# Performance work log

Measured on AMD Instinct MI355X. Metric: run time of the kernel, lower is better.

## Reference

```python
import jax, jax.numpy as jnp
import numpy as np

DIM = 1024
NUM_HEADS = 16
HEAD_DIM = DIM // NUM_HEADS
SCALE = HEAD_DIM ** -0.5


def setup_inputs() -> dict:
    key = jax.random.key(0)
    k1, k2, k3 = jax.random.split(key, 3)
    B, N = 2, 2048
    x = jax.random.normal(k1, (B, N, DIM), dtype=jnp.float32)
    # qkv: Linear(dim, 3*dim, bias=False); proj: Linear(dim, dim) with bias
    w_qkv = jax.random.normal(k2, (3 * DIM, DIM), dtype=jnp.float32) * (DIM ** -0.5)
    w_proj = jax.random.normal(k3, (DIM, DIM), dtype=jnp.float32) * (DIM ** -0.5)
    b_proj = jnp.zeros((DIM,), dtype=jnp.float32)
    return {"x": x, "w_qkv": w_qkv, "w_proj": w_proj, "b_proj": b_proj}


def reference(x, w_qkv, w_proj, b_proj):
    B, N, C = x.shape
    H, D = NUM_HEADS, HEAD_DIM
    qkv = jnp.einsum('bnc,fc->bnf', x, w_qkv)                 # [B,N,3C]
    qkv = qkv.reshape(B, N, 3, H, D).transpose(2, 0, 3, 1, 4)  # [3,B,H,N,D]
    q, k, v = qkv[0], qkv[1], qkv[2]
    q = q * SCALE
    attn = jnp.einsum('bhnd,bhmd->bhnm', q, k)                 # [B,H,N,N]
    attn = jax.nn.softmax(attn, axis=-1)
    out = jnp.einsum('bhnm,bhmd->bhnd', attn, v)               # [B,H,N,D]
    out = out.transpose(0, 2, 1, 3).reshape(B, N, C)
    out = jnp.einsum('bnc,fc->bnf', out, w_proj) + b_proj
    return out
```

## Files before the change

### kernel.cpp

```cpp
#include <hip/hip_runtime.h>
#include <hip/hip_bf16.h>
#include <stdint.h>

typedef __attribute__((ext_vector_type(4))) float f32x4;
typedef __attribute__((ext_vector_type(16))) float f32x16;
typedef __attribute__((ext_vector_type(8))) short bf16x8;
typedef __attribute__((ext_vector_type(4))) short bf16x4;
typedef unsigned short ushort_t;

#define QSCALE 0.18033688f

__device__ inline short f2bf(float f) {
  unsigned u = __builtin_bit_cast(unsigned, f);
  u += 0x7fffu + ((u >> 16) & 1u);
  return (short)(u >> 16);
}

__device__ inline void gload_lds16(const void* g, void* l) {
  __builtin_amdgcn_global_load_lds(
      (const __attribute__((address_space(1))) void*)g,
      (__attribute__((address_space(3))) void*)l, 16, 0, 0);
}

__device__ inline unsigned cvtpk(float a, float b) {
  unsigned r;
  asm("v_cvt_pk_bf16_f32 %0, %1, %2" : "=v"(r) : "v"(a), "v"(b));
  return r;
}

__device__ inline void swap32u(unsigned& a, unsigned& b) {
  asm("v_permlane32_swap_b32 %0, %1" : "+v"(a), "+v"(b));
}

__global__ __launch_bounds__(256) void cvt_all(const float* __restrict__ x,
                                               const float* __restrict__ wq,
                                               const float* __restrict__ wp,
                                               short* __restrict__ Xb,
                                               short* __restrict__ Wq,
                                               short* __restrict__ Wp) {
  int i = blockIdx.x * 256 + threadIdx.x;
  const float* s;
  short* d;
  int off;
  if (i < 524288)       { s = x;  d = Xb; off = i; }
  else if (i < 917504)  { s = wq; d = Wq; off = i - 524288; }
  else                  { s = wp; d = Wp; off = i - 917504; }
  const float4* sv = (const float4*)s;
  float4 a = sv[2 * off], b = sv[2 * off + 1];
  bf16x8 o;
  o[0] = f2bf(a.x); o[1] = f2bf(a.y); o[2] = f2bf(a.z); o[3] = f2bf(a.w);
  o[4] = f2bf(b.x); o[5] = f2bf(b.y); o[6] = f2bf(b.z); o[7] = f2bf(b.w);
  ((bf16x8*)d)[off] = o;
}

template <int F32OUT, int SPLITV, int BXPX>
__global__ __launch_bounds__(256, 2) void gemm_db(const short* __restrict__ A,
                                                  const short* __restrict__ B,
                                                  void* __restrict__ Cv,
                                                  short* __restrict__ Vtg,
                                                  const float* __restrict__ bias,
                                                  int scale_cols, float scale_val,
                                                  int M, int N, int K) {
  __shared__ char smem[65536];
  short* Ab0 = (short*)smem;
  short* Bb0 = (short*)(smem + 32768);
  const int tid = threadIdx.x, wv = tid >> 6, ln = tid & 63;
  const int wm = wv >> 1, wn = wv & 1;
  const int id = blockIdx.x;
  const int xcd = id & 7, local = id >> 3;
  const int bx = xcd * BXPX + local % BXPX;
  const int by = local / BXPX;
  const int bn0 = bx * 128, bm0 = by * 128;
  const int nt = K >> 6;

  const int srow = ln >> 3;
  const int scol = ((ln & 7) ^ (ln >> 3)) * 8;
  const int fln = ln & 15;
  const int fk = ln >> 4;

  f32x4 acc[4][4] = {};

  auto stage = [&](int t, int s) {
    const size_t k0 = (size_t)t << 6;
#pragma unroll
    for (int rd = 0; rd < 4; rd++) {
      const int ch = 4 * wv + rd;
      gload_lds16(A + (size_t)(bm0 + ch * 8 + srow) * K + k0 + scol,
                  (char*)(Ab0 + s * 8192) + ch * 1024);
      gload_lds16(B + (size_t)(bn0 + ch * 8 + srow) * K + k0 + scol,
                  (char*)(Bb0 + s * 8192) + ch * 1024);
    }
  };

  stage(0, 0);
  stage(1, 1);
  asm volatile("s_waitcnt vmcnt(8)" ::: "memory");
  __builtin_amdgcn_s_barrier();
  __builtin_amdgcn_sched_barrier(0);

  for (int t = 0; t < nt; t++) {
    const int s = t & 1;
    const char* Ap = (const char*)(Ab0 + s * 8192);
    const char* Bp = (const char*)(Bb0 + s * 8192);

    bf16x8 af[4][2], bf[4][2];
#pragma unroll
    for (int m = 0; m < 4; m++) {
      const int R = wm * 64 + m * 16 + fln;
#pragma unroll
      for (int kk = 0; kk < 2; kk++)
        af[m][kk] = *(const bf16x8*)(Ap + R * 128 + ((((kk << 2) | fk) ^ (R & 7)) << 4));
    }
#pragma unroll
    for (int n = 0; n < 4; n++) {
      const int R = wn * 64 + n * 16 + fln;
#pragma unroll
      for (int kk = 0; kk < 2; kk++)
        bf[n][kk] = *(const bf16x8*)(Bp + R * 128 + ((((kk << 2) | fk) ^ (R & 7)) << 4));
    }

    __builtin_amdgcn_s_setprio(1);
#pragma unroll
    for (int kk = 0; kk < 2; kk++)
#pragma unroll
      for (int m = 0; m < 4; m++)
#pragma unroll
        for (int n = 0; n < 4; n++)
          acc[m][n] = __builtin_amdgcn_mfma_f32_16x16x32_bf16(af[m][kk], bf[n][kk], acc[m][n], 0, 0, 0);
    __builtin_amdgcn_s_setprio(0);

    if (t + 1 < nt) {
      __builtin_amdgcn_s_barrier();
      if (t + 2 < nt) {
        stage(t + 2, s);
        asm volatile("s_waitcnt vmcnt(8)" ::: "memory");
      } else {
        asm volatile("s_waitcnt vmcnt(0)" ::: "memory");
      }
      __builtin_amdgcn_s_barrier();
      __builtin_amdgcn_sched_barrier(0);
    }
  }

  if constexpr (SPLITV) {
    if (bn0 >= 2048) {
      __syncthreads();
      short* Vl = (short*)smem;
#pragma unroll
      for (int m = 0; m < 4; m++) {
        const int tok0 = wm * 64 + m * 16 + fk * 4;
#pragma unroll
        for (int n = 0; n < 4; n++) {
          const int f_loc = wn * 64 + n * 16 + fln;
          bf16x4 w;
#pragma unroll
          for (int j = 0; j < 4; j++) w[j] = f2bf(acc[m][n][j]);
          *(bf16x4*)(Vl + f_loc * 136 + tok0) = w;
        }
      }
      __syncthreads();
      const int fbase = bn0 - 2048, bb = bm0 >> 11, ntok0 = bm0 & 2047;
#pragma unroll
      for (int pass = 0; pass < 8; pass++) {
        const int f_loc = wv * 32 + pass * 4 + (ln >> 4);
        const int f = fbase + f_loc;
        const int g = (bb * 16 + (f >> 6)) * 64 + (f & 63);
        bf16x8 w = *(const bf16x8*)(Vl + f_loc * 136 + (ln & 15) * 8);
        *(bf16x8*)(Vtg + (size_t)g * 2048 + ntok0 + (ln & 15) * 8) = w;
      }
      return;
    }
  }

  const int r0 = bm0 + wm * 64, c0 = bn0 + wn * 64;
  const int fg4 = fk * 4;
#pragma unroll
  for (int m = 0; m < 4; m++) {
    const int row0 = r0 + m * 16 + fg4;
#pragma unroll
    for (int n = 0; n < 4; n++) {
      const int col = c0 + n * 16 + fln;
      if constexpr (SPLITV) {
        const float sc = (col < scale_cols) ? scale_val : 1.0f;
#pragma unroll
        for (int j = 0; j < 4; j++)
          ((short*)Cv)[(size_t)(row0 + j) * 2048 + col] = f2bf(acc[m][n][j] * sc);
      } else {
#pragma unroll
        for (int j = 0; j < 4; j++) {
          float v = acc[m][n][j];
          if (col < scale_cols) v *= scale_val;
          if (F32OUT) ((float*)Cv)[(size_t)(row0 + j) * N + col] = v + bias[col];
          else        ((short*)Cv)[(size_t)(row0 + j) * N + col] = f2bf(v);
        }
      }
    }
  }
}

__global__ __launch_bounds__(256, 2) void attn_fwd(const short* __restrict__ QK,
                                                   const short* __restrict__ Vtg,
                                                   short* __restrict__ AO) {
  __shared__ short Ks[2][64 * 64];
  __shared__ short Vt[2][64 * 64];
  const int tid = threadIdx.x, wv = tid >> 6, ln = tid & 63;
  const int lq = ln & 31, hi = ln >> 5;
  const int id = blockIdx.x;
  const int c = (id & 7) * 64 + (id >> 3);
  const int qt = c & 15, bh = c >> 4;
  const int b = bh >> 4, h = bh & 15;
  const short* base = QK + (size_t)(b * 2048) * 2048 + h * 64;
  const short* Kg = base + 1024;
  const short* Vg = Vtg + (size_t)bh * 64 * 2048;
  const int qrow = qt * 128 + wv * 32 + lq;

  bf16x8 qf[4];
  {
    const short* Qrow = base + (size_t)qrow * 2048;
#pragma unroll
    for (int ds = 0; ds < 4; ds++)
      qf[ds] = *(const bf16x8*)(Qrow + ds * 16 + hi * 8);
  }

  bf16x8 onesf;
#pragma unroll
  for (int i = 0; i < 8; i++) onesf[i] = (short)0x3F80;

  const int krow = ln >> 3;
  const int kcol = ((ln & 7) ^ (ln >> 3)) * 8;

  f32x16 o0 = {}, o1 = {}, lacc = {};

#define STAGE(t, s)                                                              \
  {                                                                              \
    _Pragma("unroll")                                                            \
    for (int rd = 0; rd < 2; rd++) {                                             \
      const int r8 = 16 * wv + 8 * rd + krow;                                    \
      gload_lds16(Kg + (size_t)((t) * 64 + r8) * 2048 + kcol,                    \
                  (char*)Ks[s] + (2 * wv + rd) * 1024);                          \
      gload_lds16(Vg + (size_t)r8 * 2048 + (t) * 64 + kcol,                      \
                  (char*)Vt[s] + (2 * wv + rd) * 1024);                          \
    }                                                                            \
  }

  STAGE(0, 0);
  __syncthreads();

  for (int t = 0; t < 32; t++) {
    const int s = t & 1;
    if (t < 31) STAGE(t + 1, s ^ 1);

    f32x16 c0 = {}, c1 = {};
    const char* Kb = (const char*)Ks[s];
    __builtin_amdgcn_s_setprio(1);
#pragma unroll
    for (int ds = 0; ds < 4; ds++) {
      const int cp = (ds * 2 + hi) ^ (lq & 7);
      bf16x8 ka0 = *(const bf16x8*)(Kb + lq * 128 + cp * 16);
      bf16x8 ka1 = *(const bf16x8*)(Kb + (32 + lq) * 128 + cp * 16);
      c0 = __builtin_amdgcn_mfma_f32_32x32x16_bf16(ka0, qf[ds], c0, 0, 0, 0);
      c1 = __builtin_amdgcn_mfma_f32_32x32x16_bf16(ka1, qf[ds], c1, 0, 0, 0);
    }
    __builtin_amdgcn_s_setprio(0);

#pragma unroll
    for (int r = 0; r < 16; r++) c0[r] = __builtin_amdgcn_exp2f(c0[r]);
#pragma unroll
    for (int r = 0; r < 16; r++) c1[r] = __builtin_amdgcn_exp2f(c1[r]);

    bf16x8 pa[4];
#pragma unroll
    for (int cs = 0; cs < 2; cs++) {
      const f32x16& p = cs ? c1 : c0;
#pragma unroll
      for (int ksl = 0; ksl < 2; ksl++) {
        unsigned A0 = cvtpk(p[8 * ksl + 0], p[8 * ksl + 1]);
        unsigned A1 = cvtpk(p[8 * ksl + 2], p[8 * ksl + 3]);
        unsigned B0 = cvtpk(p[8 * ksl + 4], p[8 * ksl + 5]);
        unsigned B1 = cvtpk(p[8 * ksl + 6], p[8 * ksl + 7]);
        swap32u(A0, B0);
        swap32u(A1, B1);
        union { unsigned u[4]; bf16x8 v; } tmp;
        tmp.u[0] = A0; tmp.u[1] = A1; tmp.u[2] = B0; tmp.u[3] = B1;
        pa[cs * 2 + ksl] = tmp.v;
      }
    }

    const char* Vb = (const char*)Vt[s];
    __builtin_amdgcn_s_setprio(1);
#pragma unroll
    for (int ks = 0; ks < 4; ks++) {
      const int cp = (ks * 2 + hi) ^ (lq & 7);
      bf16x8 va0 = *(const bf16x8*)(Vb + lq * 128 + cp * 16);
      bf16x8 va1 = *(const bf16x8*)(Vb + (32 + lq) * 128 + cp * 16);
      o0 = __builtin_amdgcn_mfma_f32_32x32x16_bf16(va0, pa[ks], o0, 0, 0, 0);
      o1 = __builtin_amdgcn_mfma_f32_32x32x16_bf16(va1, pa[ks], o1, 0, 0, 0);
      lacc = __builtin_amdgcn_mfma_f32_32x32x16_bf16(onesf, pa[ks], lacc, 0, 0, 0);
    }
    __builtin_amdgcn_s_setprio(0);

    __syncthreads();
  }
#undef STAGE

  const float inv = __builtin_amdgcn_rcpf(lacc[0]);
  short* Arow = AO + ((size_t)(b * 2048) + qrow) * 1024 + h * 64;
#pragma unroll
  for (int dt = 0; dt < 2; dt++) {
    const f32x16& o = dt ? o1 : o0;
#pragma unroll
    for (int g = 0; g < 4; g++) {
      bf16x4 w;
#pragma unroll
      for (int i = 0; i < 4; i++) w[i] = f2bf(o[4 * g + i] * inv);
      *(bf16x4*)(Arow + dt * 32 + 8 * g + 4 * hi) = w;
    }
  }
}

extern "C" void kernel_launch(void* const* d_in, const int* in_sizes, int n_in,
                              void* d_out, int out_size, void* d_ws, size_t ws_size,
                              hipStream_t stream) {
  const float* x = (const float*)d_in[0];
  const float* w_qkv = (const float*)d_in[1];
  const float* w_proj = (const float*)d_in[2];
  const float* b_proj = (const float*)d_in[3];
  float* out = (float*)d_out;

  char* ws = (char*)d_ws;
  short* Xb  = (short*)(ws + 0);
  short* Wq  = (short*)(ws + 8388608);
  short* Wp  = (short*)(ws + 14680064);
  short* QK  = (short*)(ws + 16777216);
  short* Vtg = (short*)(ws + 33554432);
  short* AO  = (short*)(ws + 41943040);

  cvt_all<<<4096, 256, 0, stream>>>(x, w_qkv, w_proj, Xb, Wq, Wp);

  gemm_db<0, 1, 3><<<dim3(768), 256, 0, stream>>>(Xb, Wq, QK, Vtg, nullptr,
                                                  1024, QSCALE, 4096, 3072, 1024);

  attn_fwd<<<dim3(512), 256, 0, stream>>>(QK, Vtg, AO);

  gemm_db<1, 0, 1><<<dim3(256), 256, 0, stream>>>(AO, Wp, out, nullptr, b_proj,
                                                  0, 1.0f, 4096, 1024, 1024);
}
```

Baseline: 103.8 us.

## Software-pipeline attention loop: overlap QK^T of tile t with PV of tile t-1

Restructures the attention inner loop so the QK^T MFMAs for the current KV tile are issued before the exp/pack/PV work of the previous tile, carrying the score tiles across iterations. A third LDS buffer is added so the previous V tile stays resident while the next tile is being loaded. The aim is to let the exp and conversion ALU work overlap with matrix-core work and hide its latency. In exchange it costs extra registers for the carried scores and 50% more LDS, which may reduce occupancy under the 2-blocks-per-CU launch bound. The setprio hint around the PV MFMAs is also dropped.

After: 103.5 us. Within noise of the previous version (-0.4%).

```diff
diff --git a/kernel.cpp b/kernel.cpp
--- a/kernel.cpp
+++ b/kernel.cpp
@@ -201,8 +201,8 @@
 __global__ __launch_bounds__(256, 2) void attn_fwd(const short* __restrict__ QK,
                                                    const short* __restrict__ Vtg,
                                                    short* __restrict__ AO) {
-  __shared__ short Ks[2][64 * 64];
-  __shared__ short Vt[2][64 * 64];
+  __shared__ short Ks[3][64 * 64];
+  __shared__ short Vt[3][64 * 64];
   const int tid = threadIdx.x, wv = tid >> 6, ln = tid & 63;
   const int lq = ln & 31, hi = ln >> 5;
   const int id = blockIdx.x;
@@ -230,6 +230,7 @@
   const int kcol = ((ln & 7) ^ (ln >> 3)) * 8;
 
   f32x16 o0 = {}, o1 = {}, lacc = {};
+  f32x16 cp0, cp1;
 
 #define STAGE(t, s)                                                              \
   {                                                                              \
@@ -243,15 +244,49 @@
     }                                                                            \
   }
 
+#define FINISH_PV(vs)                                                            \
+  {                                                                              \
+    _Pragma("unroll")                                                            \
+    for (int r = 0; r < 16; r++) cp0[r] = __builtin_amdgcn_exp2f(cp0[r]);        \
+    _Pragma("unroll")                                                            \
+    for (int r = 0; r < 16; r++) cp1[r] = __builtin_amdgcn_exp2f(cp1[r]);        \
+    bf16x8 pa[4];                                                                \
+    _Pragma("unroll")                                                            \
+    for (int cs = 0; cs < 2; cs++) {                                             \
+      const f32x16& p = cs ? cp1 : cp0;                                          \
+      _Pragma("unroll")                                                          \
+      for (int ksl = 0; ksl < 2; ksl++) {                                        \
+        unsigned A0 = cvtpk(p[8 * ksl + 0], p[8 * ksl + 1]);                     \
+        unsigned A1 = cvtpk(p[8 * ksl + 2], p[8 * ksl + 3]);                     \
+        unsigned B0 = cvtpk(p[8 * ksl + 4], p[8 * ksl + 5]);                     \
+        unsigned B1 = cvtpk(p[8 * ksl + 6], p[8 * ksl + 7]);                     \
+        swap32u(A0, B0);                                                         \
+        swap32u(A1, B1);                                                         \
+        union { unsigned u[4]; bf16x8 v; } tmp;                                  \
+        tmp.u[0] = A0; tmp.u[1] = A1; tmp.u[2] = B0; tmp.u[3] = B1;              \
+        pa[cs * 2 + ksl] = tmp.v;                                                \
+      }                                                                          \
+    }                                                                            \
+    const char* Vb = (const char*)Vt[vs];                                        \
+    _Pragma("unroll")                                                            \
+    for (int ks = 0; ks < 4; ks++) {                                             \
+      const int cp = (ks * 2 + hi) ^ (lq & 7);                                   \
+      bf16x8 va0 = *(const bf16x8*)(Vb + lq * 128 + cp * 16);                    \
+      bf16x8 va1 = *(const bf16x8*)(Vb + (32 + lq) * 128 + cp * 16);             \
+      o0 = __builtin_amdgcn_mfma_f32_32x32x16_bf16(va0, pa[ks], o0, 0, 0, 0);    \
+      o1 = __builtin_amdgcn_mfma_f32_32x32x16_bf16(va1, pa[ks], o1, 0, 0, 0);    \
+      lacc = __builtin_amdgcn_mfma_f32_32x32x16_bf16(onesf, pa[ks], lacc, 0, 0, 0); \
+    }                                                                            \
+  }
+
   STAGE(0, 0);
   __syncthreads();
 
   for (int t = 0; t < 32; t++) {
-    const int s = t & 1;
-    if (t < 31) STAGE(t + 1, s ^ 1);
+    if (t < 31) STAGE(t + 1, (t + 1) % 3);
 
     f32x16 c0 = {}, c1 = {};
-    const char* Kb = (const char*)Ks[s];
+    const char* Kb = (const char*)Ks[t % 3];
     __builtin_amdgcn_s_setprio(1);
 #pragma unroll
     for (int ds = 0; ds < 4; ds++) {
@@ -263,44 +298,16 @@
     }
     __builtin_amdgcn_s_setprio(0);
 
-#pragma unroll
-    for (int r = 0; r < 16; r++) c0[r] = __builtin_amdgcn_exp2f(c0[r]);
-#pragma unroll
-    for (int r = 0; r < 16; r++) c1[r] = __builtin_amdgcn_exp2f(c1[r]);
-
-    bf16x8 pa[4];
-#pragma unroll
-    for (int cs = 0; cs < 2; cs++) {
-      const f32x16& p = cs ? c1 : c0;
-#pragma unroll
-      for (int ksl = 0; ksl < 2; ksl++) {
-        unsigned A0 = cvtpk(p[8 * ksl + 0], p[8 * ksl + 1]);
-        unsigned A1 = cvtpk(p[8 * ksl + 2], p[8 * ksl + 3]);
-        unsigned B0 = cvtpk(p[8 * ksl + 4], p[8 * ksl + 5]);
-        unsigned B1 = cvtpk(p[8 * ksl + 6], p[8 * ksl + 7]);
-        swap32u(A0, B0);
-        swap32u(A1, B1);
-        union { unsigned u[4]; bf16x8 v; } tmp;
-        tmp.u[0] = A0; tmp.u[1] = A1; tmp.u[2] = B0; tmp.u[3] = B1;
-        pa[cs * 2 + ksl] = tmp.v;
-      }
-    }
-
-    const char* Vb = (const char*)Vt[s];
-    __builtin_amdgcn_s_setprio(1);
-#pragma unroll
-    for (int ks = 0; ks < 4; ks++) {
-      const int cp = (ks * 2 + hi) ^ (lq & 7);
-      bf16x8 va0 = *(const bf16x8*)(Vb + lq * 128 + cp * 16);
-      bf16x8 va1 = *(const bf16x8*)(Vb + (32 + lq) * 128 + cp * 16);
-      o0 = __builtin_amdgcn_mfma_f32_32x32x16_bf16(va0, pa[ks], o0, 0, 0, 0);
-      o1 = __builtin_amdgcn_mfma_f32_32x32x16_bf16(va1, pa[ks], o1, 0, 0, 0);
-      lacc = __builtin_amdgcn_mfma_f32_32x32x16_bf16(onesf, pa[ks], lacc, 0, 0, 0);
-    }
-    __builtin_amdgcn_s_setprio(0);
-
+    if (t > 0) {
+      FINISH_PV((t - 1) % 3);
+    }
+
+    cp0 = c0;
+    cp1 = c1;
     __syncthreads();
   }
+  FINISH_PV(31 % 3);
+#undef FINISH_PV
 #undef STAGE
 
   const float inv = __builtin_amdgcn_rcpf(lacc[0]);
```
